# Kernel optimization log

Measured on AMD Instinct MI355X. Metric: run time of the kernel, lower is better.

## Reference

```python
import jax, jax.numpy as jnp
import numpy as np

N_HEAD = 12
N_EMBD = 768
N_EMBD_SIDE = 384
N_EMBD_KQ = 192
N_EMBD_OUT = N_EMBD + N_EMBD_SIDE  # 1152
B, L = 2, 2048


def setup_inputs() -> dict:
    key = jax.random.key(0)
    ks = jax.random.split(key, 12)
    s = 0.02
    return {
        "x": jax.random.normal(ks[0], (B, L, N_EMBD), dtype=jnp.float32),
        "side": jax.random.normal(ks[1], (B, L, N_EMBD_SIDE), dtype=jnp.float32),
        # weights stored as (in_features, out_features) so y = x @ W + b
        "Wq": jax.random.normal(ks[2], (N_EMBD_SIDE, N_EMBD_KQ), dtype=jnp.float32) * s,
        "bq": jnp.zeros((N_EMBD_KQ,), dtype=jnp.float32),
        "Wkv": jax.random.normal(ks[3], (N_EMBD_OUT, N_EMBD_KQ + N_EMBD_OUT), dtype=jnp.float32) * s,
        "bkv": jnp.zeros((N_EMBD_KQ + N_EMBD_OUT,), dtype=jnp.float32),
        "Wproj": jax.random.normal(ks[4], (N_EMBD_OUT, N_EMBD_OUT), dtype=jnp.float32) * s,
        "bproj": jnp.zeros((N_EMBD_OUT,), dtype=jnp.float32),
        "Wemb": jax.random.normal(ks[5], (N_EMBD_SIDE, N_EMBD_OUT), dtype=jnp.float32) * s,
        "bemb": jnp.zeros((N_EMBD_OUT,), dtype=jnp.float32),
    }


def reference(x, side, Wq, bq, Wkv, bkv, Wproj, bproj, Wemb, bemb):
    batch, length, _ = x.shape
    hd_kq = N_EMBD_KQ // N_HEAD   # 16
    hd_v = N_EMBD_OUT // N_HEAD   # 96

    q = (side @ Wq + bq).reshape(batch, length, N_HEAD, hd_kq).transpose(0, 2, 1, 3)  # [B,H,L,dk]
    kv = jnp.concatenate((x, side), axis=2) @ Wkv + bkv
    k = kv[:, :, :N_EMBD_KQ].reshape(batch, length, N_HEAD, hd_kq).transpose(0, 2, 1, 3)
    v = kv[:, :, N_EMBD_KQ:].reshape(batch, length, N_HEAD, hd_v).transpose(0, 2, 1, 3)

    first = (side[:, 0] @ Wemb + bemb).reshape(batch, N_HEAD, 1, hd_v)  # [B,H,1,dv]

    # shifted causal mask: row i attends to j < i; row 0 copies row 1 (attends to j==0)
    mask = jnp.tril(jnp.ones((length, length), dtype=bool), k=-1)
    mask = mask.at[0].set(mask[1])

    scale = 1.0 / jnp.sqrt(jnp.asarray(hd_kq, dtype=q.dtype))
    scores = jnp.einsum("bhqd,bhkd->bhqk", q, k) * scale
    scores = jnp.where(mask, scores, -jnp.inf)
    attn = jax.nn.softmax(scores, axis=-1)
    y = jnp.einsum("bhqk,bhkd->bhqd", attn, v)  # [B,H,L,dv]

    # special-case first token: replaced by learned embedding of side[:,0]
    y = jnp.concatenate((first, y[:, :, 1:]), axis=2)
    y = y.transpose(0, 2, 1, 3).reshape(batch, length, N_EMBD_OUT)
    return y @ Wproj + bproj
```

## Files before the change

### kernel.cpp

```cpp
#include <hip/hip_runtime.h>
#include <hip/hip_bf16.h>
#include <math.h>

#define N_HEADS 12
#define L_SEQ   2048
#define BATCH   2
#define D_KQ    192
#define D_OUT   1152
#define D_KV    1344
#define D_X     768
#define D_SIDE  384
#define HD_K    16
#define HD_V    96
#define M_ROWS  4096

typedef __attribute__((ext_vector_type(8))) short bf16x8;
typedef __attribute__((ext_vector_type(4))) float f32x4;

__device__ inline float  b2f(ushort u){ union{uint i; float f;} v; v.i=(uint)u<<16; return v.f; }
__device__ inline ushort f2b(float f){ __hip_bfloat16 h = __float2bfloat16(f);
                                       return *reinterpret_cast<ushort*>(&h); }

__device__ inline void gload_lds16(const ushort* g, ushort* l) {
    __builtin_amdgcn_global_load_lds(
        (const __attribute__((address_space(1))) void*)g,
        (__attribute__((address_space(3))) void*)l, 16, 0, 0);
}

#define SWZ(r, c) ((((r) * 64) + (c)) ^ (((r) & 7) << 3))

__global__ __launch_bounds__(256)
void cvt_f32_bf16(const float* __restrict__ src, int sstride,
                  ushort* __restrict__ dst, int dstride, int w4, int rows) {
    int gid = blockIdx.x * 256 + threadIdx.x;
    if (gid >= w4 * rows) return;
    int r = gid / w4, c = gid - r * w4;
    float4 v = *reinterpret_cast<const float4*>(&src[(size_t)r * sstride + c * 4]);
    ushort4 o = make_ushort4(f2b(v.x), f2b(v.y), f2b(v.z), f2b(v.w));
    *reinterpret_cast<ushort4*>(&dst[(size_t)r * dstride + c * 4]) = o;
}

__global__ __launch_bounds__(256)
void transpose_cvt(const float* __restrict__ W, ushort* __restrict__ Wt,
                   int K, int N, int Npad) {
    __shared__ float t[32][33];
    const int n0 = blockIdx.x * 32, k0 = blockIdx.y * 32;
    const int tx = threadIdx.x & 31, ty = threadIdx.x >> 5;
#pragma unroll
    for (int i = 0; i < 4; i++) {
        int n = n0 + tx;
        t[ty + i * 8][tx] = (n < N) ? W[(size_t)(k0 + ty + i * 8) * N + n] : 0.f;
    }
    __syncthreads();
#pragma unroll
    for (int i = 0; i < 4; i++) {
        int n = n0 + ty + i * 8;
        Wt[(size_t)n * K + k0 + tx] = f2b(t[tx][ty + i * 8]);
    }
}

template<int MODE>
__global__ __launch_bounds__(256)
void gemm_mfma(const ushort* __restrict__ A, const ushort* __restrict__ Bt,
               const float* __restrict__ bias, void* __restrict__ Cv,
               ushort* __restrict__ vt, int M, int N, int K) {
    __shared__ ushort As[128 * 32];
    __shared__ ushort Bs[128 * 32];
    const int tid = threadIdx.x;
    const int w = tid >> 6, lane = tid & 63;
    const int wr = w >> 1, wc = w & 1;
    const int n0 = blockIdx.x * 128, m0 = blockIdx.y * 128;
    const int l4 = lane & 3, lrow = lane >> 2;
    const int kgrp = lane >> 4, l16 = lane & 15;

    f32x4 acc[4][4];
#pragma unroll
    for (int i = 0; i < 4; i++)
#pragma unroll
        for (int j = 0; j < 4; j++)
            acc[i][j] = (f32x4){0.f, 0.f, 0.f, 0.f};

    for (int kt = 0; kt < K; kt += 32) {
        __syncthreads();
#pragma unroll
        for (int r = 0; r < 2; r++) {
            const int seg = r * 4 + w;
            const int trow = seg * 16 + lrow;
            gload_lds16(&A [(size_t)(m0 + trow) * K + kt + l4 * 8], &As[seg * 512]);
            gload_lds16(&Bt[(size_t)(n0 + trow) * K + kt + l4 * 8], &Bs[seg * 512]);
        }
        __syncthreads();

        bf16x8 a[4], b[4];
#pragma unroll
        for (int i = 0; i < 4; i++)
            a[i] = *reinterpret_cast<const bf16x8*>(
                &As[(wr * 64 + i * 16 + l16) * 32 + kgrp * 8]);
#pragma unroll
        for (int j = 0; j < 4; j++)
            b[j] = *reinterpret_cast<const bf16x8*>(
                &Bs[(wc * 64 + j * 16 + l16) * 32 + kgrp * 8]);
#pragma unroll
        for (int i = 0; i < 4; i++)
#pragma unroll
            for (int j = 0; j < 4; j++)
                acc[i][j] = __builtin_amdgcn_mfma_f32_16x16x32_bf16(
                    a[i], b[j], acc[i][j], 0, 0, 0);
    }

    const int rgrp = lane >> 4;
#pragma unroll
    for (int j = 0; j < 4; j++) {
        const int col = n0 + wc * 64 + j * 16 + l16;
        if (col >= N) continue;
        const float bv = bias[col];
        if constexpr (MODE == 2) {
            if (col >= D_KQ) {
                const int hh = (col - D_KQ) / HD_V;
                const int dd = (col - D_KQ) % HD_V;
                const int bb = m0 >> 11;
                ushort* vrow = vt + ((size_t)(bb * N_HEADS + hh) * HD_V + dd) * L_SEQ
                                  + (m0 & 2047);
#pragma unroll
                for (int i = 0; i < 4; i++) {
                    const int r0 = wr * 64 + i * 16 + rgrp * 4;
                    ushort4 o = make_ushort4(
                        f2b(acc[i][j][0] + bv), f2b(acc[i][j][1] + bv),
                        f2b(acc[i][j][2] + bv), f2b(acc[i][j][3] + bv));
                    *reinterpret_cast<ushort4*>(&vrow[r0]) = o;
                }
                continue;
            }
#pragma unroll
            for (int i = 0; i < 4; i++) {
                const int row0 = m0 + wr * 64 + i * 16 + rgrp * 4;
#pragma unroll
                for (int rg = 0; rg < 4; rg++)
                    ((ushort*)Cv)[(size_t)(row0 + rg) * D_KQ + col] =
                        f2b(acc[i][j][rg] + bv);
            }
            continue;
        }
#pragma unroll
        for (int i = 0; i < 4; i++) {
            const int row0 = m0 + wr * 64 + i * 16 + rgrp * 4;
#pragma unroll
            for (int rg = 0; rg < 4; rg++) {
                float v = acc[i][j][rg] + bv;
                if (MODE == 1)
                    ((ushort*)Cv)[(size_t)(row0 + rg) * N + col] = f2b(v);
                else
                    ((float*)Cv)[(size_t)(row0 + rg) * N + col] = v;
            }
        }
    }
}

__global__ __launch_bounds__(256)
void attn_mfma(const ushort* __restrict__ qbuf, const ushort* __restrict__ kb,
               const ushort* __restrict__ vtg, ushort* __restrict__ yb) {
    __shared__ ushort Vt[96 * 64];
    __shared__ ushort Ks[64 * 16];
    __shared__ __align__(16) ushort Kz[8];
    __shared__ ushort Ps[4][16 * 64];

    const int tid = threadIdx.x;
    const int w = tid >> 6, lane = tid & 63;
    const int l16 = lane & 15, kgrp = lane >> 4;

    const int i = blockIdx.x, jj5 = i & 255, g = i >> 8;
    const int q5 = jj5 & 31;
    const int qt = (g == 0) ? q5 : (g == 1) ? (31 - q5) : ((q5 + 16) & 31);
    const int hb = g * 8 + (jj5 >> 5);
    const int h = hb % N_HEADS, b = hb / N_HEADS;

    if (tid < 8) Kz[tid] = 0;

    const ushort* vt_h  = vtg + (size_t)(b * N_HEADS + h) * HD_V * L_SEQ;
    const ushort* kbase = kb + (size_t)b * L_SEQ * D_KQ;
    const int rowbase = qt * 64;

    int voff[3];
#pragma unroll
    for (int s3 = 0; s3 < 3; s3++) {
        const int L = (w * 3 + s3) * 1024 + lane * 16;
        const int X = L ^ (((L >> 7) & 7) << 4);
        voff[s3] = (X >> 7) * L_SEQ + ((X >> 1) & 63);
    }
    int koff = 0;
    if (w < 2) {
        const int elem = (w * 1024 + lane * 16) >> 1;
        koff = (elem >> 4) * D_KQ + h * HD_K + ((elem >> 3) & 1) * 8;
    }

    bf16x8 qf = {0, 0, 0, 0, 0, 0, 0, 0};
    if (kgrp < 2)
        qf = *reinterpret_cast<const bf16x8*>(
            qbuf + ((size_t)b * L_SEQ + rowbase + w * 16 + l16) * D_KQ
                 + h * HD_K + kgrp * 8);

    float m[4] = {-INFINITY, -INFINITY, -INFINITY, -INFINITY};
    float l[4] = {0.f, 0.f, 0.f, 0.f};
    f32x4 acc[6];
#pragma unroll
    for (int ob = 0; ob < 6; ob++) acc[ob] = (f32x4){0.f, 0.f, 0.f, 0.f};

    for (int t2 = 0; t2 <= qt; t2++) {
        const int j0 = t2 * 64;
        const bool diag = (t2 == qt);
        __syncthreads();

        if (w < 2)
            gload_lds16(kbase + (size_t)j0 * D_KQ + koff, &Ks[w * 512]);
#pragma unroll
        for (int s3 = 0; s3 < 3; s3++)
            gload_lds16(vt_h + voff[s3] + j0, &Vt[(w * 3 + s3) * 512]);
        __syncthreads();

        __builtin_amdgcn_s_setprio(1);
        f32x4 s[4];
#pragma unroll
        for (int f = 0; f < 4; f++) {
            const ushort* kp = (kgrp < 2) ? &Ks[(f * 16 + l16) * 16 + kgrp * 8]
                                          : &Kz[0];
            bf16x8 kf = *reinterpret_cast<const bf16x8*>(kp);
            s[f] = __builtin_amdgcn_mfma_f32_16x16x32_bf16(
                qf, kf, (f32x4){0.f, 0.f, 0.f, 0.f}, 0, 0, 0);
        }
        __builtin_amdgcn_s_setprio(0);

#pragma unroll
        for (int f = 0; f < 4; f++)
#pragma unroll
            for (int r = 0; r < 4; r++) {
                float v = s[f][r] * 0.25f;
                if (diag) {
                    const int row64 = w * 16 + kgrp * 4 + r;
                    const int key64 = f * 16 + l16;
                    if (key64 >= row64) v = -INFINITY;
                }
                s[f][r] = v;
            }

        float scl[4];
#pragma unroll
        for (int r = 0; r < 4; r++) {
            float mt = fmaxf(fmaxf(s[0][r], s[1][r]), fmaxf(s[2][r], s[3][r]));
            mt = fmaxf(mt, __shfl_xor(mt, 1));
            mt = fmaxf(mt, __shfl_xor(mt, 2));
            mt = fmaxf(mt, __shfl_xor(mt, 4));
            mt = fmaxf(mt, __shfl_xor(mt, 8));
            const float mn = fmaxf(m[r], mt);
            scl[r] = __expf(m[r] - mn);
            m[r] = mn;
            float ps = 0.f;
#pragma unroll
            for (int f = 0; f < 4; f++) {
                float p = __expf(s[f][r] - mn);
                s[f][r] = p;
                ps += p;
            }
            ps += __shfl_xor(ps, 1);
            ps += __shfl_xor(ps, 2);
            ps += __shfl_xor(ps, 4);
            ps += __shfl_xor(ps, 8);
            l[r] = l[r] * scl[r] + ps;
        }

#pragma unroll
        for (int f = 0; f < 4; f++)
#pragma unroll
            for (int r = 0; r < 4; r++)
                Ps[w][SWZ(kgrp * 4 + r, f * 16 + l16)] = f2b(s[f][r]);
#pragma unroll
        for (int ob = 0; ob < 6; ob++)
#pragma unroll
            for (int r = 0; r < 4; r++)
                acc[ob][r] *= scl[r];

        asm volatile("s_waitcnt lgkmcnt(0)" ::: "memory");
        __builtin_amdgcn_sched_barrier(0);

        bf16x8 pa0 = *reinterpret_cast<const bf16x8*>(&Ps[w][SWZ(l16, kgrp * 8)]);
        bf16x8 pa1 = *reinterpret_cast<const bf16x8*>(&Ps[w][SWZ(l16, 32 + kgrp * 8)]);
        __builtin_amdgcn_s_setprio(1);
#pragma unroll
        for (int ob = 0; ob < 6; ob++) {
            bf16x8 vb0 = *reinterpret_cast<const bf16x8*>(&Vt[SWZ(ob * 16 + l16, kgrp * 8)]);
            bf16x8 vb1 = *reinterpret_cast<const bf16x8*>(&Vt[SWZ(ob * 16 + l16, 32 + kgrp * 8)]);
            acc[ob] = __builtin_amdgcn_mfma_f32_16x16x32_bf16(pa0, vb0, acc[ob], 0, 0, 0);
            acc[ob] = __builtin_amdgcn_mfma_f32_16x16x32_bf16(pa1, vb1, acc[ob], 0, 0, 0);
        }
        __builtin_amdgcn_s_setprio(0);
    }

#pragma unroll
    for (int r = 0; r < 4; r++) {
        const float inv = 1.f / l[r];
        ushort* dst = yb + ((size_t)b * L_SEQ + rowbase + w * 16 + kgrp * 4 + r) * D_OUT
                        + h * HD_V;
#pragma unroll
        for (int ob = 0; ob < 6; ob++)
            dst[ob * 16 + l16] = f2b(acc[ob][r] * inv);
    }
}

__global__ __launch_bounds__(128)
void first_kernel(const float* __restrict__ side, const float* __restrict__ Wemb,
                  const float* __restrict__ bemb, ushort* __restrict__ yb) {
    const int o = blockIdx.x * 128 + threadIdx.x;
    const int b = blockIdx.y;
    const float* s = side + (size_t)b * L_SEQ * D_SIDE;
    float acc = bemb[o];
    for (int k = 0; k < D_SIDE; k++)
        acc += s[k] * Wemb[(size_t)k * D_OUT + o];
    yb[(size_t)b * L_SEQ * D_OUT + o] = f2b(acc);
}

extern "C" void kernel_launch(void* const* d_in, const int* in_sizes, int n_in,
                              void* d_out, int out_size, void* d_ws, size_t ws_size,
                              hipStream_t stream) {
    const float* x     = (const float*)d_in[0];
    const float* side  = (const float*)d_in[1];
    const float* Wq    = (const float*)d_in[2];
    const float* bq    = (const float*)d_in[3];
    const float* Wkv   = (const float*)d_in[4];
    const float* bkv   = (const float*)d_in[5];
    const float* Wproj = (const float*)d_in[6];
    const float* bproj = (const float*)d_in[7];
    const float* Wemb  = (const float*)d_in[8];
    const float* bemb  = (const float*)d_in[9];
    float* out = (float*)d_out;

    char* ws = (char*)d_ws;
    ushort* xs_bf   = (ushort*)(ws + 0);
    ushort* side_bf = (ushort*)(ws + 9437184);
    ushort* wq_t    = (ushort*)(ws + 12582912);
    ushort* wkv_t   = (ushort*)(ws + 12779520);
    ushort* wproj_t = (ushort*)(ws + 16023552);
    ushort* qbuf    = (ushort*)(ws + 18677760);
    ushort* kbuf    = (ushort*)(ws + 20250624);
    ushort* vtg     = (ushort*)(ws + 21823488);
    ushort* ybuf    = (ushort*)(ws + 31260672);

    {
        int items_x  = (D_X / 4) * M_ROWS;
        int items_sd = (D_SIDE / 4) * M_ROWS;
        cvt_f32_bf16<<<(items_x  + 255) / 256, 256, 0, stream>>>(
            x,    D_X,    xs_bf,       D_OUT,  D_X / 4,    M_ROWS);
        cvt_f32_bf16<<<(items_sd + 255) / 256, 256, 0, stream>>>(
            side, D_SIDE, xs_bf + D_X, D_OUT,  D_SIDE / 4, M_ROWS);
        cvt_f32_bf16<<<(items_sd + 255) / 256, 256, 0, stream>>>(
            side, D_SIDE, side_bf,     D_SIDE, D_SIDE / 4, M_ROWS);
    }
    transpose_cvt<<<dim3(8, 12),  256, 0, stream>>>(Wq,    wq_t,    D_SIDE, D_KQ,  256);
    transpose_cvt<<<dim3(44, 36), 256, 0, stream>>>(Wkv,   wkv_t,   D_OUT,  D_KV,  1408);
    transpose_cvt<<<dim3(36, 36), 256, 0, stream>>>(Wproj, wproj_t, D_OUT,  D_OUT, 1152);

    gemm_mfma<1><<<dim3(2, 32),  256, 0, stream>>>(
        side_bf, wq_t, bq, qbuf, nullptr, M_ROWS, D_KQ, D_SIDE);
    gemm_mfma<2><<<dim3(11, 32), 256, 0, stream>>>(
        xs_bf, wkv_t, bkv, kbuf, vtg, M_ROWS, D_KV, D_OUT);
    attn_mfma<<<768, 256, 0, stream>>>(qbuf, kbuf, vtg, ybuf);
    first_kernel<<<dim3(9, BATCH), 128, 0, stream>>>(side, Wemb, bemb, ybuf);
    gemm_mfma<0><<<dim3(9, 32),  256, 0, stream>>>(
        ybuf, wproj_t, bproj, out, nullptr, M_ROWS, D_OUT, D_OUT);
}
```

Before: 280.1 us.

## Fuse Q projection into KV GEMM, merge conversions, use 32-row attention tiles

The Q projection is folded into the KV GEMM. Wq is appended as extra output columns of a combined transposed weight, zero-padded over the x rows of K, and the epilogue routes those columns to qbuf with bq. The three input conversion kernels become one, and the Wq transpose and separate Q GEMM are removed, which cuts launches and the extra side_bf buffer. Attention now uses 2-warp blocks over 32-row query tiles, doubling the grid for better causal load balance, with per-tile diagonal masking offsets. The trade-off is wasted MFMA work on the zero-padded Wq region and more K/V tile reloads per query row.

Result: faster. 259.0 us (-7.5%).

```diff
diff --git a/kernel.cpp b/kernel.cpp
--- a/kernel.cpp
+++ b/kernel.cpp
@@ -8,6 +8,7 @@
 #define D_KQ    192
 #define D_OUT   1152
 #define D_KV    1344
+#define D_KVQ   1536
 #define D_X     768
 #define D_SIDE  384
 #define HD_K    16
@@ -17,7 +18,6 @@
 typedef __attribute__((ext_vector_type(8))) short bf16x8;
 typedef __attribute__((ext_vector_type(4))) float f32x4;
 
-__device__ inline float  b2f(ushort u){ union{uint i; float f;} v; v.i=(uint)u<<16; return v.f; }
 __device__ inline ushort f2b(float f){ __hip_bfloat16 h = __float2bfloat16(f);
                                        return *reinterpret_cast<ushort*>(&h); }
 
@@ -30,31 +30,59 @@
 #define SWZ(r, c) ((((r) * 64) + (c)) ^ (((r) & 7) << 3))
 
 __global__ __launch_bounds__(256)
-void cvt_f32_bf16(const float* __restrict__ src, int sstride,
-                  ushort* __restrict__ dst, int dstride, int w4, int rows) {
-    int gid = blockIdx.x * 256 + threadIdx.x;
-    if (gid >= w4 * rows) return;
-    int r = gid / w4, c = gid - r * w4;
-    float4 v = *reinterpret_cast<const float4*>(&src[(size_t)r * sstride + c * 4]);
-    ushort4 o = make_ushort4(f2b(v.x), f2b(v.y), f2b(v.z), f2b(v.w));
-    *reinterpret_cast<ushort4*>(&dst[(size_t)r * dstride + c * 4]) = o;
+void cvt_inputs(const float* __restrict__ x, const float* __restrict__ side,
+                ushort* __restrict__ xs_bf) {
+    const int gid = blockIdx.x * 256 + threadIdx.x;
+    if (gid < 786432) {
+        const int r = gid / 192, c = (gid - r * 192) * 4;
+        float4 v = *reinterpret_cast<const float4*>(&x[(size_t)r * D_X + c]);
+        ushort4 o = make_ushort4(f2b(v.x), f2b(v.y), f2b(v.z), f2b(v.w));
+        *reinterpret_cast<ushort4*>(&xs_bf[(size_t)r * D_OUT + c]) = o;
+    } else {
+        const int g2 = gid - 786432;
+        const int r = g2 / 96, c = (g2 - r * 96) * 4;
+        float4 v = *reinterpret_cast<const float4*>(&side[(size_t)r * D_SIDE + c]);
+        ushort4 o = make_ushort4(f2b(v.x), f2b(v.y), f2b(v.z), f2b(v.w));
+        *reinterpret_cast<ushort4*>(&xs_bf[(size_t)r * D_OUT + D_X + c]) = o;
+    }
 }
 
 __global__ __launch_bounds__(256)
-void transpose_cvt(const float* __restrict__ W, ushort* __restrict__ Wt,
-                   int K, int N, int Npad) {
+void transpose_kvq(const float* __restrict__ Wkv, const float* __restrict__ Wq,
+                   ushort* __restrict__ Wt) {
     __shared__ float t[32][33];
     const int n0 = blockIdx.x * 32, k0 = blockIdx.y * 32;
     const int tx = threadIdx.x & 31, ty = threadIdx.x >> 5;
 #pragma unroll
     for (int i = 0; i < 4; i++) {
-        int n = n0 + tx;
-        t[ty + i * 8][tx] = (n < N) ? W[(size_t)(k0 + ty + i * 8) * N + n] : 0.f;
+        const int k = k0 + ty + i * 8, n = n0 + tx;
+        float v;
+        if (n < D_KV)        v = Wkv[(size_t)k * D_KV + n];
+        else if (k >= D_X)   v = Wq[(size_t)(k - D_X) * D_KQ + (n - D_KV)];
+        else                 v = 0.f;
+        t[ty + i * 8][tx] = v;
     }
     __syncthreads();
 #pragma unroll
     for (int i = 0; i < 4; i++) {
-        int n = n0 + ty + i * 8;
+        const int n = n0 + ty + i * 8;
+        Wt[(size_t)n * D_OUT + k0 + tx] = f2b(t[tx][ty + i * 8]);
+    }
+}
+
+__global__ __launch_bounds__(256)
+void transpose_cvt(const float* __restrict__ W, ushort* __restrict__ Wt,
+                   int K, int N) {
+    __shared__ float t[32][33];
+    const int n0 = blockIdx.x * 32, k0 = blockIdx.y * 32;
+    const int tx = threadIdx.x & 31, ty = threadIdx.x >> 5;
+#pragma unroll
+    for (int i = 0; i < 4; i++)
+        t[ty + i * 8][tx] = W[(size_t)(k0 + ty + i * 8) * N + n0 + tx];
+    __syncthreads();
+#pragma unroll
+    for (int i = 0; i < 4; i++) {
+        const int n = n0 + ty + i * 8;
         Wt[(size_t)n * K + k0 + tx] = f2b(t[tx][ty + i * 8]);
     }
 }
@@ -62,8 +90,9 @@
 template<int MODE>
 __global__ __launch_bounds__(256)
 void gemm_mfma(const ushort* __restrict__ A, const ushort* __restrict__ Bt,
-               const float* __restrict__ bias, void* __restrict__ Cv,
-               ushort* __restrict__ vt, int M, int N, int K) {
+               const float* __restrict__ bias, const float* __restrict__ bias2,
+               void* __restrict__ Cv, ushort* __restrict__ vt,
+               ushort* __restrict__ qout, int M, int N, int K) {
     __shared__ ushort As[128 * 32];
     __shared__ ushort Bs[128 * 32];
     const int tid = threadIdx.x;
@@ -112,10 +141,19 @@
 #pragma unroll
     for (int j = 0; j < 4; j++) {
         const int col = n0 + wc * 64 + j * 16 + l16;
-        if (col >= N) continue;
-        const float bv = bias[col];
         if constexpr (MODE == 2) {
-            if (col >= D_KQ) {
+            if (col < D_KQ) {
+                const float bv = bias[col];
+#pragma unroll
+                for (int i = 0; i < 4; i++) {
+                    const int row0 = m0 + wr * 64 + i * 16 + rgrp * 4;
+#pragma unroll
+                    for (int rg = 0; rg < 4; rg++)
+                        ((ushort*)Cv)[(size_t)(row0 + rg) * D_KQ + col] =
+                            f2b(acc[i][j][rg] + bv);
+                }
+            } else if (col < D_KV) {
+                const float bv = bias[col];
                 const int hh = (col - D_KQ) / HD_V;
                 const int dd = (col - D_KQ) % HD_V;
                 const int bb = m0 >> 11;
@@ -129,66 +167,67 @@
                         f2b(acc[i][j][2] + bv), f2b(acc[i][j][3] + bv));
                     *reinterpret_cast<ushort4*>(&vrow[r0]) = o;
                 }
-                continue;
-            }
-#pragma unroll
-            for (int i = 0; i < 4; i++) {
-                const int row0 = m0 + wr * 64 + i * 16 + rgrp * 4;
-#pragma unroll
-                for (int rg = 0; rg < 4; rg++)
-                    ((ushort*)Cv)[(size_t)(row0 + rg) * D_KQ + col] =
-                        f2b(acc[i][j][rg] + bv);
+            } else {
+                const int qc = col - D_KV;
+                const float bv = bias2[qc];
+#pragma unroll
+                for (int i = 0; i < 4; i++) {
+                    const int row0 = m0 + wr * 64 + i * 16 + rgrp * 4;
+#pragma unroll
+                    for (int rg = 0; rg < 4; rg++)
+                        qout[(size_t)(row0 + rg) * D_KQ + qc] =
+                            f2b(acc[i][j][rg] + bv);
+                }
             }
             continue;
         }
+        if (col >= N) continue;
+        const float bv = bias[col];
 #pragma unroll
         for (int i = 0; i < 4; i++) {
             const int row0 = m0 + wr * 64 + i * 16 + rgrp * 4;
 #pragma unroll
-            for (int rg = 0; rg < 4; rg++) {
-                float v = acc[i][j][rg] + bv;
-                if (MODE == 1)
-                    ((ushort*)Cv)[(size_t)(row0 + rg) * N + col] = f2b(v);
-                else
-                    ((float*)Cv)[(size_t)(row0 + rg) * N + col] = v;
-            }
-        }
-    }
-}
-
-__global__ __launch_bounds__(256)
+            for (int rg = 0; rg < 4; rg++)
+                ((float*)Cv)[(size_t)(row0 + rg) * N + col] = acc[i][j][rg] + bv;
+        }
+    }
+}
+
+__global__ __launch_bounds__(128)
 void attn_mfma(const ushort* __restrict__ qbuf, const ushort* __restrict__ kb,
                const ushort* __restrict__ vtg, ushort* __restrict__ yb) {
     __shared__ ushort Vt[96 * 64];
     __shared__ ushort Ks[64 * 16];
     __shared__ __align__(16) ushort Kz[8];
-    __shared__ ushort Ps[4][16 * 64];
+    __shared__ ushort Ps[2][16 * 64];
 
     const int tid = threadIdx.x;
     const int w = tid >> 6, lane = tid & 63;
     const int l16 = lane & 15, kgrp = lane >> 4;
 
-    const int i = blockIdx.x, jj5 = i & 255, g = i >> 8;
-    const int q5 = jj5 & 31;
-    const int qt = (g == 0) ? q5 : (g == 1) ? (31 - q5) : ((q5 + 16) & 31);
-    const int hb = g * 8 + (jj5 >> 5);
+    const int i = blockIdx.x, j5 = i & 255, g = i >> 8;
+    const int tb = j5 & 63;
+    const int t  = (g & 1) ? (63 - tb) : tb;
+    const int hb = (g << 2) | (j5 >> 6);
     const int h = hb % N_HEADS, b = hb / N_HEADS;
 
     if (tid < 8) Kz[tid] = 0;
 
     const ushort* vt_h  = vtg + (size_t)(b * N_HEADS + h) * HD_V * L_SEQ;
     const ushort* kbase = kb + (size_t)b * L_SEQ * D_KQ;
-    const int rowbase = qt * 64;
-
-    int voff[3];
-#pragma unroll
-    for (int s3 = 0; s3 < 3; s3++) {
-        const int L = (w * 3 + s3) * 1024 + lane * 16;
+    const int rowbase = t * 32;
+    const int nt = (t >> 1) + 1;
+    const int rowoff = (t & 1) * 32;
+
+    int voff[6];
+#pragma unroll
+    for (int s6 = 0; s6 < 6; s6++) {
+        const int L = (w * 6 + s6) * 1024 + lane * 16;
         const int X = L ^ (((L >> 7) & 7) << 4);
-        voff[s3] = (X >> 7) * L_SEQ + ((X >> 1) & 63);
-    }
-    int koff = 0;
-    if (w < 2) {
+        voff[s6] = (X >> 7) * L_SEQ + ((X >> 1) & 63);
+    }
+    int koff;
+    {
         const int elem = (w * 1024 + lane * 16) >> 1;
         koff = (elem >> 4) * D_KQ + h * HD_K + ((elem >> 3) & 1) * 8;
     }
@@ -205,16 +244,15 @@
 #pragma unroll
     for (int ob = 0; ob < 6; ob++) acc[ob] = (f32x4){0.f, 0.f, 0.f, 0.f};
 
-    for (int t2 = 0; t2 <= qt; t2++) {
+    for (int t2 = 0; t2 < nt; t2++) {
         const int j0 = t2 * 64;
-        const bool diag = (t2 == qt);
+        const bool diag = (t2 == nt - 1);
         __syncthreads();
 
-        if (w < 2)
-            gload_lds16(kbase + (size_t)j0 * D_KQ + koff, &Ks[w * 512]);
-#pragma unroll
-        for (int s3 = 0; s3 < 3; s3++)
-            gload_lds16(vt_h + voff[s3] + j0, &Vt[(w * 3 + s3) * 512]);
+        gload_lds16(kbase + (size_t)j0 * D_KQ + koff, &Ks[w * 512]);
+#pragma unroll
+        for (int s6 = 0; s6 < 6; s6++)
+            gload_lds16(vt_h + voff[s6] + j0, &Vt[(w * 6 + s6) * 512]);
         __syncthreads();
 
         __builtin_amdgcn_s_setprio(1);
@@ -235,9 +273,9 @@
             for (int r = 0; r < 4; r++) {
                 float v = s[f][r] * 0.25f;
                 if (diag) {
-                    const int row64 = w * 16 + kgrp * 4 + r;
+                    const int row32 = w * 16 + kgrp * 4 + r;
                     const int key64 = f * 16 + l16;
-                    if (key64 >= row64) v = -INFINITY;
+                    if (key64 >= rowoff + row32) v = -INFINITY;
                 }
                 s[f][r] = v;
             }
@@ -334,35 +372,24 @@
 
     char* ws = (char*)d_ws;
     ushort* xs_bf   = (ushort*)(ws + 0);
-    ushort* side_bf = (ushort*)(ws + 9437184);
-    ushort* wq_t    = (ushort*)(ws + 12582912);
-    ushort* wkv_t   = (ushort*)(ws + 12779520);
-    ushort* wproj_t = (ushort*)(ws + 16023552);
-    ushort* qbuf    = (ushort*)(ws + 18677760);
-    ushort* kbuf    = (ushort*)(ws + 20250624);
-    ushort* vtg     = (ushort*)(ws + 21823488);
-    ushort* ybuf    = (ushort*)(ws + 31260672);
-
-    {
-        int items_x  = (D_X / 4) * M_ROWS;
-        int items_sd = (D_SIDE / 4) * M_ROWS;
-        cvt_f32_bf16<<<(items_x  + 255) / 256, 256, 0, stream>>>(
-            x,    D_X,    xs_bf,       D_OUT,  D_X / 4,    M_ROWS);
-        cvt_f32_bf16<<<(items_sd + 255) / 256, 256, 0, stream>>>(
-            side, D_SIDE, xs_bf + D_X, D_OUT,  D_SIDE / 4, M_ROWS);
-        cvt_f32_bf16<<<(items_sd + 255) / 256, 256, 0, stream>>>(
-            side, D_SIDE, side_bf,     D_SIDE, D_SIDE / 4, M_ROWS);
-    }
-    transpose_cvt<<<dim3(8, 12),  256, 0, stream>>>(Wq,    wq_t,    D_SIDE, D_KQ,  256);
-    transpose_cvt<<<dim3(44, 36), 256, 0, stream>>>(Wkv,   wkv_t,   D_OUT,  D_KV,  1408);
-    transpose_cvt<<<dim3(36, 36), 256, 0, stream>>>(Wproj, wproj_t, D_OUT,  D_OUT, 1152);
-
-    gemm_mfma<1><<<dim3(2, 32),  256, 0, stream>>>(
-        side_bf, wq_t, bq, qbuf, nullptr, M_ROWS, D_KQ, D_SIDE);
-    gemm_mfma<2><<<dim3(11, 32), 256, 0, stream>>>(
-        xs_bf, wkv_t, bkv, kbuf, vtg, M_ROWS, D_KV, D_OUT);
-    attn_mfma<<<768, 256, 0, stream>>>(qbuf, kbuf, vtg, ybuf);
+    ushort* wkvq_t  = (ushort*)(ws + 9437184);
+    ushort* wproj_t = (ushort*)(ws + 12976128);
+    ushort* qbuf    = (ushort*)(ws + 15630336);
+    ushort* kbuf    = (ushort*)(ws + 17203200);
+    ushort* vtg     = (ushort*)(ws + 18776064);
+    ushort* ybuf    = (ushort*)(ws + 28213248);
+
+    cvt_inputs<<<4608, 256, 0, stream>>>(x, side, xs_bf);
+    transpose_kvq<<<dim3(48, 36), 256, 0, stream>>>(Wkv, Wq, wkvq_t);
+    transpose_cvt<<<dim3(36, 36), 256, 0, stream>>>(Wproj, wproj_t, D_OUT, D_OUT);
+
+    gemm_mfma<2><<<dim3(12, 32), 256, 0, stream>>>(
+        xs_bf, wkvq_t, bkv, bq, kbuf, vtg, qbuf, M_ROWS, D_KVQ, D_OUT);
+
+    attn_mfma<<<1536, 128, 0, stream>>>(qbuf, kbuf, vtg, ybuf);
+
     first_kernel<<<dim3(9, BATCH), 128, 0, stream>>>(side, Wemb, bemb, ybuf);
-    gemm_mfma<0><<<dim3(9, 32),  256, 0, stream>>>(
-        ybuf, wproj_t, bproj, out, nullptr, M_ROWS, D_OUT, D_OUT);
-}
+
+    gemm_mfma<0><<<dim3(9, 32), 256, 0, stream>>>(
+        ybuf, wproj_t, bproj, nullptr, out, nullptr, nullptr, M_ROWS, D_OUT, D_OUT);
+}
```
